# Optimization experiments

Measured on AMD Instinct MI355X. Metric: run time of the kernel, lower is better.

Reference implementation:

```python
import jax, jax.numpy as jnp
import numpy as np

EPS = 1e-5  # F.normalize eps


def _l2norm(x):
    # torch F.normalize(p=2): x / max(||x||, eps)
    n = jnp.sqrt(jnp.sum(x * x, axis=-1, keepdims=True))
    return x / jnp.maximum(n, EPS)


def setup_inputs() -> dict:
    B, L, D, T = 32, 128, 256, 10000
    key = jax.random.key(0)
    ks = jax.random.split(key, 10)
    data = jax.random.normal(ks[0], (B, L, D), jnp.float32)
    # event ids in [1, T]; 0 is the padding id (none here, so packing matches original loop)
    event_type = jax.random.randint(ks[1], (B, L), 1, T + 1, dtype=jnp.int32)
    emb_table = jax.random.normal(ks[2], (T + 1, D), jnp.float32)
    place_correlation = jax.random.uniform(ks[3], (T, T), jnp.float32)
    xav = np.sqrt(2.0 / (T + D))  # xavier_normal_ std for Linear(dim, num_types)
    W5 = jax.random.normal(ks[4], (T, D), jnp.float32) * xav
    W1 = jax.random.normal(ks[5], (T, D), jnp.float32) * xav
    W2 = jax.random.normal(ks[6], (T, D), jnp.float32) * xav
    W3 = jax.random.normal(ks[7], (T, D), jnp.float32) * xav
    W4 = jax.random.normal(ks[8], (T, D), jnp.float32) * xav
    one = jnp.ones((1,), jnp.float32)
    # F.dropout(p=0.5, training=True): precomputed keep-mask already scaled by 1/(1-p)=2
    drop_mask = jax.random.bernoulli(ks[9], 0.5, (B, L, T)).astype(jnp.float32) * 2.0
    return dict(data=data, event_type=event_type, emb_table=emb_table,
                place_correlation=place_correlation, W1=W1, W2=W2, W3=W3, W4=W4,
                W5=W5, a=one, b=one, c=one, d=one, drop_mask=drop_mask)


def reference(data, event_type, emb_table, place_correlation,
              W1, W2, W3, W4, W5, a, b, c, d, drop_mask):
    B = data.shape[0]
    T = W5.shape[0]
    # event_emb(event_type).detach()
    event_enc = jax.lax.stop_gradient(emb_table[event_type])           # [B,L,D]
    inner = jnp.tanh(jnp.einsum('bld,td->blt', event_enc, W5)) * drop_mask  # [B,L,T]
    valid = event_type != 0                                            # pad mask
    idx = jnp.where(valid, event_type - 1, 0)                          # [B,L]
    # per-event gather of correlation rows, fused multiply + reduce over L
    corr = place_correlation[idx] * valid[..., None].astype(place_correlation.dtype)  # [B,L,T]
    item = _l2norm(jnp.sum(inner * corr, axis=1))                      # [B,T]
    # target_: ones, zeroed at observed event indices
    rows = jnp.arange(B)[:, None]
    target = jnp.ones((B, T), jnp.float32).at[rows, idx].min(
        jnp.where(valid, 0.0, 1.0).astype(jnp.float32))
    dm = jnp.mean(data, axis=1)                                        # [B,D]
    p = lambda W: _l2norm(dm @ W.T)
    out = jnp.tanh(p(W1) * a + p(W2) * b + p(W3) * c + p(W4) * d + item)
    return out, target
```

## Files before the change

kernel.cpp:

```cpp
#include <hip/hip_runtime.h>
#include <hip/hip_bf16.h>
#include <stdint.h>

#define T_DIM 10000
#define B_DIM 32
#define L_DIM 128
#define D_DIM 256
#define NT_TILES 79
#define TPAD (NT_TILES*128)

typedef __bf16 bf16x8 __attribute__((ext_vector_type(8)));
typedef float  f32x4  __attribute__((ext_vector_type(4)));
typedef unsigned short us8 __attribute__((ext_vector_type(8)));
typedef unsigned short ushort_t;

__device__ __forceinline__ unsigned short f2bf(float f){
  union { float f; uint32_t u; } v; v.f = f;
  uint32_t u = v.u;
  return (unsigned short)((u + 0x7fffu + ((u >> 16) & 1u)) >> 16);
}

__device__ __forceinline__ void async16(const void* g, void* l){
  __builtin_amdgcn_global_load_lds((const __attribute__((address_space(1))) void*)g,
                                   (__attribute__((address_space(3))) void*)l,
                                   16, 0, 0);
}

__device__ __forceinline__ float fast_tanh(float x){
  x = fminf(8.f, fmaxf(-8.f, x));
  float e = __expf(2.f * x);
  return (e - 1.f) * __builtin_amdgcn_rcpf(e + 1.f);
}

__global__ __launch_bounds__(64) void k_gather_emb(const float* __restrict__ emb,
    const int* __restrict__ et, ushort_t* __restrict__ ebf){
  int r = blockIdx.x;
  int d4 = threadIdx.x;
  int e = et[r];
  float4 v = *((const float4*)(emb + (size_t)e * D_DIM) + d4);
  ushort4 o; o.x = f2bf(v.x); o.y = f2bf(v.y); o.z = f2bf(v.z); o.w = f2bf(v.w);
  *((ushort4*)(ebf + (size_t)r * D_DIM) + d4) = o;
}

__global__ __launch_bounds__(64) void k_conv_w5(const float* __restrict__ W5,
                                                ushort_t* __restrict__ w5b){
  int t = blockIdx.x;
  int d4 = threadIdx.x;
  ushort4 o = {0,0,0,0};
  if (t < T_DIM){
    float4 v = *((const float4*)(W5 + (size_t)t * D_DIM) + d4);
    o.x = f2bf(v.x); o.y = f2bf(v.y); o.z = f2bf(v.z); o.w = f2bf(v.w);
  }
  *((ushort4*)(w5b + (size_t)t * D_DIM) + d4) = o;
}

__global__ __launch_bounds__(256) void k_dm(const float* __restrict__ data,
                                            ushort_t* __restrict__ dmb){
  int b = blockIdx.x, d = threadIdx.x;
  const float* p = data + (size_t)b * L_DIM * D_DIM + d;
  float s = 0.f;
  #pragma unroll 4
  for (int l = 0; l < L_DIM; l++) s += p[(size_t)l * D_DIM];
  dmb[b * D_DIM + d] = f2bf(s * (1.0f / L_DIM));
}

__global__ __launch_bounds__(256) void k_big(
    const ushort_t* __restrict__ ebf, const ushort_t* __restrict__ w5b,
    const float* __restrict__ corr, const float* __restrict__ drop,
    const int* __restrict__ et, float* __restrict__ item){
  __shared__ __align__(16) ushort_t lA[128 * 128];
  __shared__ __align__(16) ushort_t lB[128 * 128];
  const int b  = blockIdx.y;
  const int t0 = blockIdx.x * 128;
  const int tid = threadIdx.x;
  const int w = tid >> 6, lane = tid & 63, col = lane & 15, quad = lane >> 4;

  f32x4 zero4 = {0.f, 0.f, 0.f, 0.f};
  f32x4 acc[2][8];
  #pragma unroll
  for (int m = 0; m < 2; m++)
    #pragma unroll
    for (int n = 0; n < 8; n++) acc[m][n] = zero4;

  for (int c = 0; c < 2; c++){
    if (c) __syncthreads();
    #pragma unroll
    for (int r = 0; r < 8; r++){
      int row = r * 16 + w * 4 + quad;
      int gseg = col ^ (row & 7);
      async16(ebf + (size_t)(b * L_DIM + row) * D_DIM + c * 128 + gseg * 8,
              lA + (r * 16 + w * 4) * 128);
      async16(w5b + (size_t)(t0 + row) * D_DIM + c * 128 + gseg * 8,
              lB + (r * 16 + w * 4) * 128);
    }
    __syncthreads();
    #pragma unroll
    for (int kk = 0; kk < 4; kk++){
      bf16x8 af[2];
      #pragma unroll
      for (int m = 0; m < 2; m++){
        int row = (w * 2 + m) * 16 + col;
        int sg = (kk * 4 + quad) ^ (row & 7);
        af[m] = *(const bf16x8*)(lA + row * 128 + sg * 8);
      }
      #pragma unroll
      for (int n = 0; n < 8; n++){
        int row = n * 16 + col;
        int sg = (kk * 4 + quad) ^ (row & 7);
        bf16x8 bf = *(const bf16x8*)(lB + row * 128 + sg * 8);
        acc[0][n] = __builtin_amdgcn_mfma_f32_16x16x32_bf16(af[0], bf, acc[0][n], 0, 0, 0);
        acc[1][n] = __builtin_amdgcn_mfma_f32_16x16x32_bf16(af[1], bf, acc[1][n], 0, 0, 0);
      }
    }
  }
  __syncthreads();

  const float* dptr[8]; const float* cptr[8]; float vm[8];
  #pragma unroll
  for (int m = 0; m < 2; m++)
    #pragma unroll
    for (int j = 0; j < 4; j++){
      int i = m * 4 + j;
      int l = (w * 2 + m) * 16 + quad * 4 + j;
      int e = et[b * L_DIM + l];
      dptr[i] = drop + (size_t)(b * L_DIM + l) * T_DIM;
      cptr[i] = corr + (size_t)(e > 0 ? e - 1 : 0) * T_DIM;
      vm[i] = (e > 0) ? 1.f : 0.f;
    }

  float* red = (float*)lA;
  #pragma unroll
  for (int n = 0; n < 8; n++){
    int t = t0 + n * 16 + col;
    bool tv = t < T_DIM;
    float s = 0.f;
    #pragma unroll
    for (int m = 0; m < 2; m++)
      #pragma unroll
      for (int j = 0; j < 4; j++){
        int i = m * 4 + j;
        float th = fast_tanh(acc[m][n][j]);
        float dv = tv ? dptr[i][t] : 0.f;
        float cv = tv ? cptr[i][t] : 0.f;
        s += th * dv * (cv * vm[i]);
      }
    s += __shfl_xor(s, 16);
    s += __shfl_xor(s, 32);
    if (lane < 16) red[w * 128 + n * 16 + col] = s;
  }
  __syncthreads();
  if (tid < 128){
    int t = t0 + tid;
    if (t < T_DIM)
      item[(size_t)b * T_DIM + t] = red[tid] + red[128 + tid] + red[256 + tid] + red[384 + tid];
  }
}

__global__ __launch_bounds__(256) void k_qgemm(
    const float* __restrict__ W1, const float* __restrict__ W2,
    const float* __restrict__ W3, const float* __restrict__ W4,
    const ushort_t* __restrict__ dmb, float* __restrict__ q){
  __shared__ __align__(16) ushort_t lB[128 * 128];
  const int kw = blockIdx.y;
  const float* W = (kw == 0) ? W1 : (kw == 1) ? W2 : (kw == 2) ? W3 : W4;
  const int t0 = blockIdx.x * 128;
  const int tid = threadIdx.x;
  const int w = tid >> 6, lane = tid & 63, col = lane & 15, quad = lane >> 4;

  f32x4 zero4 = {0.f, 0.f, 0.f, 0.f};
  f32x4 acc[2][2];
  acc[0][0] = zero4; acc[0][1] = zero4; acc[1][0] = zero4; acc[1][1] = zero4;

  for (int c = 0; c < 2; c++){
    if (c) __syncthreads();
    #pragma unroll
    for (int it = 0; it < 8; it++){
      int idx = it * 256 + tid;
      int row = idx >> 4, slot = idx & 15;
      int gseg = slot ^ (row & 7);
      int t = t0 + row;
      float4 u0 = {0,0,0,0}, u1 = {0,0,0,0};
      if (t < T_DIM){
        const float* gp = W + (size_t)t * D_DIM + c * 128 + gseg * 8;
        u0 = *(const float4*)gp;
        u1 = *(const float4*)(gp + 4);
      }
      us8 o;
      o[0] = f2bf(u0.x); o[1] = f2bf(u0.y); o[2] = f2bf(u0.z); o[3] = f2bf(u0.w);
      o[4] = f2bf(u1.x); o[5] = f2bf(u1.y); o[6] = f2bf(u1.z); o[7] = f2bf(u1.w);
      *(us8*)(lB + row * 128 + slot * 8) = o;
    }
    __syncthreads();
    #pragma unroll
    for (int kk = 0; kk < 4; kk++){
      int kabs = c * 128 + kk * 32 + quad * 8;
      bf16x8 af[2];
      #pragma unroll
      for (int m = 0; m < 2; m++)
        af[m] = *(const bf16x8*)(dmb + (size_t)(m * 16 + col) * D_DIM + kabs);
      #pragma unroll
      for (int n2 = 0; n2 < 2; n2++){
        int row = (w * 2 + n2) * 16 + col;
        int sg = (kk * 4 + quad) ^ (row & 7);
        bf16x8 bf = *(const bf16x8*)(lB + row * 128 + sg * 8);
        acc[0][n2] = __builtin_amdgcn_mfma_f32_16x16x32_bf16(af[0], bf, acc[0][n2], 0, 0, 0);
        acc[1][n2] = __builtin_amdgcn_mfma_f32_16x16x32_bf16(af[1], bf, acc[1][n2], 0, 0, 0);
      }
    }
  }
  #pragma unroll
  for (int m = 0; m < 2; m++)
    #pragma unroll
    for (int n2 = 0; n2 < 2; n2++)
      #pragma unroll
      for (int j = 0; j < 4; j++){
        int brow = m * 16 + quad * 4 + j;
        int t = t0 + (w * 2 + n2) * 16 + col;
        if (t < T_DIM)
          q[((size_t)kw * B_DIM + brow) * T_DIM + t] = acc[m][n2][j];
      }
}

__global__ __launch_bounds__(256) void k_norms(const float* __restrict__ q,
    const float* __restrict__ item, float* __restrict__ norms){
  int which = blockIdx.x, b = blockIdx.y;
  const float* src = (which < 4) ? (q + ((size_t)which * B_DIM + b) * T_DIM)
                                 : (item + (size_t)b * T_DIM);
  float s = 0.f;
  for (int i = threadIdx.x; i < T_DIM; i += 256){ float v = src[i]; s = fmaf(v, v, s); }
  #pragma unroll
  for (int o = 1; o < 64; o <<= 1) s += __shfl_xor(s, o);
  __shared__ float tmp[4];
  if ((threadIdx.x & 63) == 0) tmp[threadIdx.x >> 6] = s;
  __syncthreads();
  if (threadIdx.x == 0) norms[which * B_DIM + b] = sqrtf(tmp[0] + tmp[1] + tmp[2] + tmp[3]);
}

__global__ __launch_bounds__(256) void k_final(
    const float* __restrict__ q, const float* __restrict__ item,
    const float* __restrict__ norms,
    const float* __restrict__ pa, const float* __restrict__ pb,
    const float* __restrict__ pc, const float* __restrict__ pd,
    float* __restrict__ out, float* __restrict__ tgt){
  int b = blockIdx.y;
  int t = blockIdx.x * 256 + threadIdx.x;
  if (t >= T_DIM) return;
  float coef0 = *pa, coef1 = *pb, coef2 = *pc, coef3 = *pd;
  float v = item[(size_t)b * T_DIM + t] / fmaxf(norms[4 * B_DIM + b], 1e-5f);
  v += q[((size_t)0 * B_DIM + b) * T_DIM + t] * coef0 / fmaxf(norms[0 * B_DIM + b], 1e-5f);
  v += q[((size_t)1 * B_DIM + b) * T_DIM + t] * coef1 / fmaxf(norms[1 * B_DIM + b], 1e-5f);
  v += q[((size_t)2 * B_DIM + b) * T_DIM + t] * coef2 / fmaxf(norms[2 * B_DIM + b], 1e-5f);
  v += q[((size_t)3 * B_DIM + b) * T_DIM + t] * coef3 / fmaxf(norms[3 * B_DIM + b], 1e-5f);
  out[(size_t)b * T_DIM + t] = tanhf(v);
  tgt[(size_t)b * T_DIM + t] = 1.0f;
}

__global__ __launch_bounds__(256) void k_scatter(const int* __restrict__ et,
                                                 float* __restrict__ tgt){
  int i = blockIdx.x * 256 + threadIdx.x;
  if (i < B_DIM * L_DIM){
    int e = et[i];
    if (e > 0) tgt[(size_t)(i >> 7) * T_DIM + (e - 1)] = 0.f;
  }
}

extern "C" void kernel_launch(void* const* d_in, const int* in_sizes, int n_in,
                              void* d_out, int out_size, void* d_ws, size_t ws_size,
                              hipStream_t stream){
  const float* data = (const float*)d_in[0];
  const int*   et   = (const int*)d_in[1];
  const float* emb  = (const float*)d_in[2];
  const float* corr = (const float*)d_in[3];
  const float* W1   = (const float*)d_in[4];
  const float* W2   = (const float*)d_in[5];
  const float* W3   = (const float*)d_in[6];
  const float* W4   = (const float*)d_in[7];
  const float* W5   = (const float*)d_in[8];
  const float* ca   = (const float*)d_in[9];
  const float* cb   = (const float*)d_in[10];
  const float* cc   = (const float*)d_in[11];
  const float* cd   = (const float*)d_in[12];
  const float* drop = (const float*)d_in[13];

  char* p = (char*)d_ws;
  ushort_t* ebf  = (ushort_t*)p; p += (size_t)B_DIM * L_DIM * D_DIM * 2;
  ushort_t* w5b  = (ushort_t*)p; p += (size_t)TPAD * D_DIM * 2;
  ushort_t* dmb  = (ushort_t*)p; p += (size_t)B_DIM * D_DIM * 2;
  float*    q    = (float*)p;    p += (size_t)4 * B_DIM * T_DIM * 4;
  float*    item = (float*)p;    p += (size_t)B_DIM * T_DIM * 4;
  float*    norms= (float*)p;    p += (size_t)5 * B_DIM * 4;

  float* out = (float*)d_out;
  float* tgt = out + (size_t)B_DIM * T_DIM;

  hipLaunchKernelGGL(k_gather_emb, dim3(B_DIM * L_DIM), dim3(64), 0, stream, emb, et, ebf);
  hipLaunchKernelGGL(k_conv_w5,    dim3(TPAD),          dim3(64), 0, stream, W5, w5b);
  hipLaunchKernelGGL(k_dm,         dim3(B_DIM),         dim3(256), 0, stream, data, dmb);
  hipLaunchKernelGGL(k_big,        dim3(NT_TILES, B_DIM), dim3(256), 0, stream,
                     ebf, w5b, corr, drop, et, item);
  hipLaunchKernelGGL(k_qgemm,      dim3(NT_TILES, 4),   dim3(256), 0, stream,
                     W1, W2, W3, W4, dmb, q);
  hipLaunchKernelGGL(k_norms,      dim3(5, B_DIM),      dim3(256), 0, stream, q, item, norms);
  hipLaunchKernelGGL(k_final,      dim3(40, B_DIM),     dim3(256), 0, stream,
                     q, item, norms, ca, cb, cc, cd, out, tgt);
  hipLaunchKernelGGL(k_scatter,    dim3(16),            dim3(256), 0, stream, et, tgt);
}
```

Baseline: 696.9 us.

## Merge prep kernels, halve k_big LDS tiles for occupancy, fold scatter into norms

Combines the three prep kernels (embedding gather, W5 conversion, data mean) and the target ones-fill into a single launch. The scatter of target zeros moves into an extra block column of k_norms, which removes two launches and lets k_final skip writing the target. k_big now stages the K dimension in 64-wide chunks over four iterations, halving LDS use, and declares a minimum of 4 blocks per CU to raise occupancy for its memory-bound epilogue. The epilogue keeps 32-bit offsets instead of 64-bit pointers to cut register use, at the cost of more barriers per tile.

```diff
diff --git a/kernel.cpp b/kernel.cpp
--- a/kernel.cpp
+++ b/kernel.cpp
@@ -32,48 +32,50 @@
   return (e - 1.f) * __builtin_amdgcn_rcpf(e + 1.f);
 }
 
-__global__ __launch_bounds__(64) void k_gather_emb(const float* __restrict__ emb,
-    const int* __restrict__ et, ushort_t* __restrict__ ebf){
-  int r = blockIdx.x;
-  int d4 = threadIdx.x;
-  int e = et[r];
-  float4 v = *((const float4*)(emb + (size_t)e * D_DIM) + d4);
-  ushort4 o; o.x = f2bf(v.x); o.y = f2bf(v.y); o.z = f2bf(v.z); o.w = f2bf(v.w);
-  *((ushort4*)(ebf + (size_t)r * D_DIM) + d4) = o;
-}
-
-__global__ __launch_bounds__(64) void k_conv_w5(const float* __restrict__ W5,
-                                                ushort_t* __restrict__ w5b){
-  int t = blockIdx.x;
-  int d4 = threadIdx.x;
-  ushort4 o = {0,0,0,0};
-  if (t < T_DIM){
-    float4 v = *((const float4*)(W5 + (size_t)t * D_DIM) + d4);
-    o.x = f2bf(v.x); o.y = f2bf(v.y); o.z = f2bf(v.z); o.w = f2bf(v.w);
-  }
-  *((ushort4*)(w5b + (size_t)t * D_DIM) + d4) = o;
-}
-
-__global__ __launch_bounds__(256) void k_dm(const float* __restrict__ data,
-                                            ushort_t* __restrict__ dmb){
-  int b = blockIdx.x, d = threadIdx.x;
-  const float* p = data + (size_t)b * L_DIM * D_DIM + d;
-  float s = 0.f;
-  #pragma unroll 4
-  for (int l = 0; l < L_DIM; l++) s += p[(size_t)l * D_DIM];
-  dmb[b * D_DIM + d] = f2bf(s * (1.0f / L_DIM));
-}
-
-__global__ __launch_bounds__(256) void k_big(
+__global__ __launch_bounds__(256) void k_prep(
+    const float* __restrict__ emb, const int* __restrict__ et,
+    const float* __restrict__ W5, const float* __restrict__ data,
+    ushort_t* __restrict__ ebf, ushort_t* __restrict__ w5b,
+    ushort_t* __restrict__ dmb, float* __restrict__ tgt){
+  int bx = blockIdx.x, tid = threadIdx.x;
+  if (bx < 1024){
+    int r = bx * 4 + (tid >> 6), d4 = tid & 63;
+    int e = et[r];
+    float4 v = *((const float4*)(emb + (size_t)e * D_DIM) + d4);
+    ushort4 o; o.x = f2bf(v.x); o.y = f2bf(v.y); o.z = f2bf(v.z); o.w = f2bf(v.w);
+    *((ushort4*)(ebf + (size_t)r * D_DIM) + d4) = o;
+  } else if (bx < 3552){
+    int r = (bx - 1024) * 4 + (tid >> 6), d4 = tid & 63;
+    ushort4 o = {0,0,0,0};
+    if (r < T_DIM){
+      float4 v = *((const float4*)(W5 + (size_t)r * D_DIM) + d4);
+      o.x = f2bf(v.x); o.y = f2bf(v.y); o.z = f2bf(v.z); o.w = f2bf(v.w);
+    }
+    *((ushort4*)(w5b + (size_t)r * D_DIM) + d4) = o;
+  } else if (bx < 3584){
+    int b = bx - 3552, d = tid;
+    const float* p = data + (size_t)b * L_DIM * D_DIM + d;
+    float s = 0.f;
+    #pragma unroll 4
+    for (int l = 0; l < L_DIM; l++) s += p[(size_t)l * D_DIM];
+    dmb[b * D_DIM + d] = f2bf(s * (1.0f / L_DIM));
+  } else {
+    int i = (bx - 3584) * 256 + tid;
+    if (i < B_DIM * T_DIM) tgt[i] = 1.0f;
+  }
+}
+
+__global__ __launch_bounds__(256, 4) void k_big(
     const ushort_t* __restrict__ ebf, const ushort_t* __restrict__ w5b,
     const float* __restrict__ corr, const float* __restrict__ drop,
     const int* __restrict__ et, float* __restrict__ item){
-  __shared__ __align__(16) ushort_t lA[128 * 128];
-  __shared__ __align__(16) ushort_t lB[128 * 128];
+  __shared__ __align__(16) ushort_t lA[128 * 64];
+  __shared__ __align__(16) ushort_t lB[128 * 64];
   const int b  = blockIdx.y;
   const int t0 = blockIdx.x * 128;
   const int tid = threadIdx.x;
   const int w = tid >> 6, lane = tid & 63, col = lane & 15, quad = lane >> 4;
+  const int srow8 = lane >> 3, sslot = lane & 7;
 
   f32x4 zero4 = {0.f, 0.f, 0.f, 0.f};
   f32x4 acc[2][8];
@@ -82,32 +84,33 @@
     #pragma unroll
     for (int n = 0; n < 8; n++) acc[m][n] = zero4;
 
-  for (int c = 0; c < 2; c++){
+  for (int c = 0; c < 4; c++){
     if (c) __syncthreads();
     #pragma unroll
-    for (int r = 0; r < 8; r++){
-      int row = r * 16 + w * 4 + quad;
-      int gseg = col ^ (row & 7);
-      async16(ebf + (size_t)(b * L_DIM + row) * D_DIM + c * 128 + gseg * 8,
-              lA + (r * 16 + w * 4) * 128);
-      async16(w5b + (size_t)(t0 + row) * D_DIM + c * 128 + gseg * 8,
-              lB + (r * 16 + w * 4) * 128);
+    for (int it = 0; it < 4; it++){
+      int rb = (it * 4 + w) * 8;
+      int row = rb + srow8;
+      int gseg = sslot ^ (row & 7);
+      async16(ebf + (size_t)(b * L_DIM + row) * D_DIM + c * 64 + gseg * 8,
+              lA + rb * 64);
+      async16(w5b + (size_t)(t0 + row) * D_DIM + c * 64 + gseg * 8,
+              lB + rb * 64);
     }
     __syncthreads();
     #pragma unroll
-    for (int kk = 0; kk < 4; kk++){
+    for (int kk = 0; kk < 2; kk++){
       bf16x8 af[2];
       #pragma unroll
       for (int m = 0; m < 2; m++){
-        int row = (w * 2 + m) * 16 + col;
+        int row = w * 32 + m * 16 + col;
         int sg = (kk * 4 + quad) ^ (row & 7);
-        af[m] = *(const bf16x8*)(lA + row * 128 + sg * 8);
+        af[m] = *(const bf16x8*)(lA + row * 64 + sg * 8);
       }
       #pragma unroll
       for (int n = 0; n < 8; n++){
         int row = n * 16 + col;
         int sg = (kk * 4 + quad) ^ (row & 7);
-        bf16x8 bf = *(const bf16x8*)(lB + row * 128 + sg * 8);
+        bf16x8 bf = *(const bf16x8*)(lB + row * 64 + sg * 8);
         acc[0][n] = __builtin_amdgcn_mfma_f32_16x16x32_bf16(af[0], bf, acc[0][n], 0, 0, 0);
         acc[1][n] = __builtin_amdgcn_mfma_f32_16x16x32_bf16(af[1], bf, acc[1][n], 0, 0, 0);
       }
@@ -115,16 +118,16 @@
   }
   __syncthreads();
 
-  const float* dptr[8]; const float* cptr[8]; float vm[8];
+  int doff[8]; int coff[8]; float vm[8];
   #pragma unroll
   for (int m = 0; m < 2; m++)
     #pragma unroll
     for (int j = 0; j < 4; j++){
       int i = m * 4 + j;
-      int l = (w * 2 + m) * 16 + quad * 4 + j;
+      int l = w * 32 + m * 16 + quad * 4 + j;
       int e = et[b * L_DIM + l];
-      dptr[i] = drop + (size_t)(b * L_DIM + l) * T_DIM;
-      cptr[i] = corr + (size_t)(e > 0 ? e - 1 : 0) * T_DIM;
+      doff[i] = (b * L_DIM + l) * T_DIM;
+      coff[i] = (e > 0 ? e - 1 : 0) * T_DIM;
       vm[i] = (e > 0) ? 1.f : 0.f;
     }
 
@@ -140,8 +143,8 @@
       for (int j = 0; j < 4; j++){
         int i = m * 4 + j;
         float th = fast_tanh(acc[m][n][j]);
-        float dv = tv ? dptr[i][t] : 0.f;
-        float cv = tv ? cptr[i][t] : 0.f;
+        float dv = tv ? drop[(size_t)doff[i] + t] : 0.f;
+        float cv = tv ? corr[(size_t)coff[i] + t] : 0.f;
         s += th * dv * (cv * vm[i]);
       }
     s += __shfl_xor(s, 16);
@@ -222,8 +225,16 @@
 }
 
 __global__ __launch_bounds__(256) void k_norms(const float* __restrict__ q,
-    const float* __restrict__ item, float* __restrict__ norms){
+    const float* __restrict__ item, float* __restrict__ norms,
+    const int* __restrict__ et, float* __restrict__ tgt){
   int which = blockIdx.x, b = blockIdx.y;
+  if (which == 5){
+    if (threadIdx.x < L_DIM){
+      int e = et[b * L_DIM + threadIdx.x];
+      if (e > 0) tgt[(size_t)b * T_DIM + (e - 1)] = 0.f;
+    }
+    return;
+  }
   const float* src = (which < 4) ? (q + ((size_t)which * B_DIM + b) * T_DIM)
                                  : (item + (size_t)b * T_DIM);
   float s = 0.f;
@@ -241,7 +252,7 @@
     const float* __restrict__ norms,
     const float* __restrict__ pa, const float* __restrict__ pb,
     const float* __restrict__ pc, const float* __restrict__ pd,
-    float* __restrict__ out, float* __restrict__ tgt){
+    float* __restrict__ out){
   int b = blockIdx.y;
   int t = blockIdx.x * 256 + threadIdx.x;
   if (t >= T_DIM) return;
@@ -252,16 +263,6 @@
   v += q[((size_t)2 * B_DIM + b) * T_DIM + t] * coef2 / fmaxf(norms[2 * B_DIM + b], 1e-5f);
   v += q[((size_t)3 * B_DIM + b) * T_DIM + t] * coef3 / fmaxf(norms[3 * B_DIM + b], 1e-5f);
   out[(size_t)b * T_DIM + t] = tanhf(v);
-  tgt[(size_t)b * T_DIM + t] = 1.0f;
-}
-
-__global__ __launch_bounds__(256) void k_scatter(const int* __restrict__ et,
-                                                 float* __restrict__ tgt){
-  int i = blockIdx.x * 256 + threadIdx.x;
-  if (i < B_DIM * L_DIM){
-    int e = et[i];
-    if (e > 0) tgt[(size_t)(i >> 7) * T_DIM + (e - 1)] = 0.f;
-  }
 }
 
 extern "C" void kernel_launch(void* const* d_in, const int* in_sizes, int n_in,
@@ -293,15 +294,14 @@
   float* out = (float*)d_out;
   float* tgt = out + (size_t)B_DIM * T_DIM;
 
-  hipLaunchKernelGGL(k_gather_emb, dim3(B_DIM * L_DIM), dim3(64), 0, stream, emb, et, ebf);
-  hipLaunchKernelGGL(k_conv_w5,    dim3(TPAD),          dim3(64), 0, stream, W5, w5b);
-  hipLaunchKernelGGL(k_dm,         dim3(B_DIM),         dim3(256), 0, stream, data, dmb);
-  hipLaunchKernelGGL(k_big,        dim3(NT_TILES, B_DIM), dim3(256), 0, stream,
+  hipLaunchKernelGGL(k_prep,  dim3(4834),            dim3(256), 0, stream,
+                     emb, et, W5, data, ebf, w5b, dmb, tgt);
+  hipLaunchKernelGGL(k_big,   dim3(NT_TILES, B_DIM), dim3(256), 0, stream,
                      ebf, w5b, corr, drop, et, item);
-  hipLaunchKernelGGL(k_qgemm,      dim3(NT_TILES, 4),   dim3(256), 0, stream,
+  hipLaunchKernelGGL(k_qgemm, dim3(NT_TILES, 4),     dim3(256), 0, stream,
                      W1, W2, W3, W4, dmb, q);
-  hipLaunchKernelGGL(k_norms,      dim3(5, B_DIM),      dim3(256), 0, stream, q, item, norms);
-  hipLaunchKernelGGL(k_final,      dim3(40, B_DIM),     dim3(256), 0, stream,
-                     q, item, norms, ca, cb, cc, cd, out, tgt);
-  hipLaunchKernelGGL(k_scatter,    dim3(16),            dim3(256), 0, stream, et, tgt);
-}
+  hipLaunchKernelGGL(k_norms, dim3(6, B_DIM),        dim3(256), 0, stream,
+                     q, item, norms, et, tgt);
+  hipLaunchKernelGGL(k_final, dim3(40, B_DIM),       dim3(256), 0, stream,
+                     q, item, norms, ca, cb, cc, cd, out);
+}
```

After: 693.1 us. Within noise of the previous version (-0.5%).
